# Performance work log

Measured on AMD Instinct MI355X. Metric: run time of the kernel, lower is better.

The kernel has to match this reference:

```python
import jax, jax.numpy as jnp
import numpy as np
from functools import partial

B, S, H = 4, 2048, 1152
NH, HD = 12, 96          # heads, head_dim
NM, MD = 4, 128          # memory heads (indices 6..9), mem_dim
K = 4                    # base kernel
STRIDE = 64              # NeuralMemory chunk stride
INNER = 4 * H            # GLU inner dim
CS_DIL = (1, 2, 4, 8, 16, 32)  # DilatedConvStack: config.dilations[:6]
HEAD_DIL = ((1, 2, 4), (1, 1, 1), (4, 8, 16), (8, 16, 32), (32, 64, 128),
            (64, 128, 256), (256, 512, 1024), (1, 100, 200), (1, 500, 1000),
            (1, 1024, 2048), (3, 9, 27), (5, 25, 125))
MEM_HEADS = (6, 7, 8, 9)


def setup_inputs() -> dict:
    key = jax.random.key(0)
    ks = iter(jax.random.split(key, 48))
    def nrm(shape, s=0.02):
        return jax.random.normal(next(ks), shape, jnp.float32) * s
    return {
        'x': jax.random.normal(next(ks), (B, S, H), jnp.float32),
        'norm1_w': jnp.ones((H,), jnp.float32),
        'norm2_w': jnp.ones((H,), jnp.float32),
        'norm3_w': jnp.ones((H,), jnp.float32),
        'cs_w': nrm((6, H, K), 0.1), 'cs_b': jnp.zeros((6, H), jnp.float32),
        'cs_proj_w': nrm((H, H)), 'cs_proj_b': jnp.zeros((H,), jnp.float32),
        'gate_proj_w': nrm((H, 2 * H)),
        'router_w': nrm((H, NH)), 'router_b': jnp.zeros((NH,), jnp.float32),
        'head_w': nrm((NH, 3, HD, K), 0.1), 'head_b': jnp.zeros((NH, 3, HD), jnp.float32),
        'mem_q': nrm((NM, HD, HD), 0.01), 'mem_k': nrm((NM, HD, HD), 0.01),
        'mem_v': nrm((NM, HD, MD), 0.01), 'mem_gw': nrm((NM, HD)),
        'mem_gb': jnp.full((NM,), -2.0, jnp.float32), 'mem_out': nrm((NM, MD, HD), 0.01),
        'mixgate_w': nrm((H, H)), 'mixgate_b': jnp.full((H,), 2.0, jnp.float32),
        'mixing_w': nrm((H, H)), 'mixing_b': jnp.zeros((H,), jnp.float32),
        'ffn_in_w': nrm((H, 2 * INNER)), 'ffn_out_w': nrm((INNER, H)),
        'cg_w': nrm((H,)), 'cg_b': jnp.float32(1.0),
        'sg_w': nrm((H,)), 'sg_b': jnp.float32(1.0),
        'fg_w': nrm((H,)), 'fg_b': jnp.float32(1.0),
    }


def rmsnorm(x, w, eps=1e-6):
    n = jax.lax.rsqrt(jnp.mean(x * x, axis=-1, keepdims=True) + eps)
    return x * n * w


def dconv(x, w, b, d):
    """Depthwise causal dilated conv. x:[B,S,C], w:[C,K], b:[C]."""
    s = x.shape[1]
    pad = (w.shape[1] - 1) * d
    xp = jnp.pad(x, ((0, 0), (pad, 0), (0, 0)))
    acc = b
    for j in range(w.shape[1]):
        acc = acc + w[:, j] * jax.lax.dynamic_slice_in_dim(xp, j * d, s, axis=1)
    return acc


def conv_stack(x, cs_w, cs_b, proj_w, proj_b):
    h = x
    for i, d in enumerate(CS_DIL):
        h = h + jax.nn.gelu(dconv(h, cs_w[i], cs_b[i], d), approximate=False)
    return h @ proj_w + proj_b


def neural_memory(xm, Wq, Wk, Wv, gw, gb, Wout):
    """Chunked fast-weight memory for NM heads at once. xm:[B,S,NM,HD]."""
    q = jnp.einsum('bsnd,nde->bsne', xm, Wq)
    k = jnp.einsum('bsnd,nde->bsne', xm, Wk)
    v = jnp.einsum('bsnd,ndm->bsnm', xm, Wv)
    g = jax.nn.sigmoid(jnp.einsum('bsnd,nd->bsn', xm, gw) + gb)[..., None]  # [B,S,NM,1]
    nC = S // STRIDE
    def chunk(a):  # [B,S,...] -> [nC,B,STRIDE,...]
        return a.reshape(B, nC, STRIDE, *a.shape[2:]).swapaxes(0, 1)
    q_c, kg_c, v_c = chunk(q), chunk(k * g), chunk(v)
    ga_c = chunk(g).mean(axis=2)[..., None]  # [nC,B,NM,1,1]
    M0 = jnp.zeros((B, NM, HD, MD), xm.dtype)
    def step(M, xs):
        qc, kc, vc, ga = xs
        reads = jnp.einsum('bsnd,bndm->bsnm', qc, M)
        write = jnp.einsum('bsnd,bsnm->bndm', kc, vc)
        return (1.0 - ga) * M + write, reads
    _, reads = jax.lax.scan(step, M0, (q_c, kg_c, v_c, ga_c))
    reads = reads.swapaxes(0, 1).reshape(B, S, NM, MD)
    return jnp.einsum('bsnm,nmd->bsnd', reads, Wout)


def multi_head_state(x, gate_proj_w, router_w, router_b, head_w, head_b,
                     mem_q, mem_k, mem_v, mem_gw, mem_gb, mem_out,
                     mixgate_w, mixgate_b, mixing_w, mixing_b):
    head_weights = jax.nn.sigmoid(x @ router_w + router_b)  # [B,S,NH]
    gp = x @ gate_proj_w
    xg = gp[..., :H] * jax.nn.sigmoid(gp[..., H:])
    xh = xg.reshape(B, S, NH, HD)
    outs = []
    for i in range(NH):
        h = xh[:, :, i, :]
        for j, d in enumerate(HEAD_DIL[i]):
            h = h + dconv(h, head_w[i, j], head_b[i, j], d)
        outs.append(h)
    mem = neural_memory(xh[:, :, MEM_HEADS[0]:MEM_HEADS[-1] + 1, :],
                        mem_q, mem_k, mem_v, mem_gw, mem_gb, mem_out)
    for n, i in enumerate(MEM_HEADS):
        outs[i] = outs[i] + mem[:, :, n, :]
    out = jnp.stack(outs, axis=2) * head_weights[..., None]
    out = out.reshape(B, S, H)
    out = out * jax.nn.sigmoid(out @ mixgate_w + mixgate_b)
    return out @ mixing_w + mixing_b


def glu(x, win, wout):
    h = x @ win
    return (h[..., :INNER] * jax.nn.sigmoid(h[..., INNER:])) @ wout


def reference(x, norm1_w, norm2_w, norm3_w, cs_w, cs_b, cs_proj_w, cs_proj_b,
              gate_proj_w, router_w, router_b, head_w, head_b,
              mem_q, mem_k, mem_v, mem_gw, mem_gb, mem_out,
              mixgate_w, mixgate_b, mixing_w, mixing_b,
              ffn_in_w, ffn_out_w, cg_w, cg_b, sg_w, sg_b, fg_w, fg_b):
    gc = jax.nn.sigmoid(x @ cg_w + cg_b)[..., None]
    x = x + gc * conv_stack(rmsnorm(x, norm1_w), cs_w, cs_b, cs_proj_w, cs_proj_b)
    gs = jax.nn.sigmoid(x @ sg_w + sg_b)[..., None]
    x = x + gs * multi_head_state(rmsnorm(x, norm2_w), gate_proj_w, router_w, router_b,
                                  head_w, head_b, mem_q, mem_k, mem_v, mem_gw, mem_gb,
                                  mem_out, mixgate_w, mixgate_b, mixing_w, mixing_b)
    gf = jax.nn.sigmoid(x @ fg_w + fg_b)[..., None]
    x = x + gf * glu(rmsnorm(x, norm3_w), ffn_in_w, ffn_out_w)
    return x
```

## Files before the change

### kernel.cpp

```cpp
#include <hip/hip_runtime.h>
#include <hip/hip_bf16.h>
#include <math.h>

#define TOKENS 8192
#define HDIM 1152
#define SEQ 2048
#define NHEADS 12
#define HEADD 96
#define NMEM 4
#define MEMD 128
#define FINNER 4608

typedef __hip_bfloat16 bf16;
typedef __attribute__((ext_vector_type(8))) short short8;
typedef __attribute__((ext_vector_type(4))) float floatx4;

__device__ __constant__ int g_hd_dil[NHEADS * 3] = {
    1, 2, 4,   1, 1, 1,    4, 8, 16,   8, 16, 32,
    32, 64, 128, 64, 128, 256, 256, 512, 1024, 1, 100, 200,
    1, 500, 1000, 1, 1024, 2048, 3, 9, 27, 5, 25, 125};

__device__ inline float sigm(float x) { return 1.0f / (1.0f + expf(-x)); }
__device__ inline float gelu_exact(float x) {
  return 0.5f * x * (1.0f + erff(x * 0.70710678118654752f));
}
__device__ inline float wred(float v) {
#pragma unroll
  for (int o = 32; o > 0; o >>= 1) v += __shfl_down(v, o);
  return v;
}
__device__ inline void gl_lds16(const bf16* g, bf16* l) {
  __builtin_amdgcn_global_load_lds(
      (const __attribute__((address_space(1))) unsigned int*)g,
      (__attribute__((address_space(3))) unsigned int*)l, 16, 0, 0);
}

__global__ __launch_bounds__(256) void k_transpose_bf16(
    const float* __restrict__ W, bf16* __restrict__ WT, int K, int N) {
  __shared__ float t[32][33];
  int k0 = blockIdx.y * 32, n0 = blockIdx.x * 32;
  int tx = threadIdx.x & 31, ty = threadIdx.x >> 5;
#pragma unroll
  for (int i = 0; i < 32; i += 8)
    t[ty + i][tx] = W[(size_t)(k0 + ty + i) * N + (n0 + tx)];
  __syncthreads();
#pragma unroll
  for (int i = 0; i < 32; i += 8)
    WT[(size_t)(n0 + ty + i) * K + (k0 + tx)] = __float2bfloat16(t[tx][ty + i]);
}

__global__ __launch_bounds__(256) void k_transpose_pair(
    const float* __restrict__ W, bf16* __restrict__ WT, int K, int N) {
  __shared__ float t[32][33];
  int half = N >> 1;
  int k0 = blockIdx.y * 32, n0 = blockIdx.x * 32;
  int tx = threadIdx.x & 31, ty = threadIdx.x >> 5;
  int c = (tx < 16) ? (n0 / 2 + tx) : (half + n0 / 2 + tx - 16);
#pragma unroll
  for (int i = 0; i < 32; i += 8)
    t[ty + i][tx] = W[(size_t)(k0 + ty + i) * N + c];
  __syncthreads();
#pragma unroll
  for (int i = 0; i < 32; i += 8) {
    int r = ty + i;
    int cc = (r >> 1) + (r & 1) * 16;
    WT[(size_t)(n0 + r) * K + (k0 + tx)] = __float2bfloat16(t[tx][cc]);
  }
}

__global__ __launch_bounds__(256) void k_rms_gate(
    const float* __restrict__ x, const float* __restrict__ nw,
    const float* __restrict__ gw, const float* __restrict__ gb,
    bf16* __restrict__ outb, float* __restrict__ gout,
    const float* __restrict__ rw, const float* __restrict__ rb,
    float* __restrict__ hwout) {
  int wave = threadIdx.x >> 6, lane = threadIdx.x & 63;
  int tok = blockIdx.x * 4 + wave;
  const float* row = x + (size_t)tok * HDIM;
  float2 a[9];
  float s2 = 0.f, gd = 0.f;
#pragma unroll
  for (int p = 0; p < 9; ++p) {
    int i2 = lane + 64 * p;
    a[p] = *reinterpret_cast<const float2*>(&row[i2 * 2]);
    float2 g2 = *reinterpret_cast<const float2*>(&gw[i2 * 2]);
    s2 += a[p].x * a[p].x + a[p].y * a[p].y;
    gd += a[p].x * g2.x + a[p].y * g2.y;
  }
  s2 = wred(s2);
  gd = wred(gd);
  if (lane == 0) gout[tok] = sigm(gd + gb[0]);
  s2 = __shfl(s2, 0);
  float rn = 1.0f / sqrtf(s2 / (float)HDIM + 1e-6f);
  float racc[NHEADS];
#pragma unroll
  for (int o = 0; o < NHEADS; ++o) racc[o] = 0.f;
#pragma unroll
  for (int p = 0; p < 9; ++p) {
    int i2 = lane + 64 * p;
    float2 w2 = *reinterpret_cast<const float2*>(&nw[i2 * 2]);
    float nx = a[p].x * rn * w2.x;
    float ny = a[p].y * rn * w2.y;
    __hip_bfloat162 pr;
    pr.x = __float2bfloat16(nx);
    pr.y = __float2bfloat16(ny);
    *reinterpret_cast<__hip_bfloat162*>(&outb[(size_t)tok * HDIM + i2 * 2]) = pr;
    if (hwout) {
      const float* rp = &rw[(size_t)(i2 * 2) * NHEADS];
#pragma unroll
      for (int o = 0; o < NHEADS; ++o)
        racc[o] += nx * rp[o] + ny * rp[NHEADS + o];
    }
  }
  if (hwout) {
#pragma unroll
    for (int o = 0; o < NHEADS; ++o) {
      float r = wred(racc[o]);
      if (lane == 0) hwout[(size_t)tok * NHEADS + o] = sigm(r + rb[o]);
    }
  }
}

#define CS_T 256
#define CS_HALO 189
#define CS_ROWS 445
#define CS_J 28
__global__ __launch_bounds__(256) void k_convstack(
    const bf16* __restrict__ hin, bf16* __restrict__ outb,
    const float* __restrict__ cw, const float* __restrict__ cb) {
  __shared__ float cur[CS_ROWS * 16];
  int bx = blockIdx.x;
  int cs = bx % 72;
  int tile = (bx / 72) & 7;
  int b = bx / 576;
  int c0 = cs * 16;
  int S0 = tile * CS_T;
  int tid = threadIdx.x;
  int c = tid & 15, pg = tid >> 4;
  for (int i = tid; i < CS_ROWS * 8; i += 256) {
    int p = i >> 3, cc2 = (i & 7) * 2;
    int sg = S0 - CS_HALO + p;
    if (sg >= 0) {
      unsigned int u = *reinterpret_cast<const unsigned int*>(
          &hin[((size_t)(b * SEQ + sg)) * HDIM + c0 + cc2]);
      cur[p * 16 + cc2] = __uint_as_float(u << 16);
      cur[p * 16 + cc2 + 1] = __uint_as_float(u & 0xffff0000u);
    } else {
      cur[p * 16 + cc2] = 0.f;
      cur[p * 16 + cc2 + 1] = 0.f;
    }
  }
  const int dil[6] = {1, 2, 4, 8, 16, 32};
  const int Nk[6] = {3, 9, 21, 45, 93, 189};
  float nv[CS_J];
#pragma unroll
  for (int k = 0; k < 6; ++k) {
    int d = dil[k];
    float w0 = cw[((size_t)k * HDIM + c0 + c) * 4 + 0];
    float w1 = cw[((size_t)k * HDIM + c0 + c) * 4 + 1];
    float w2 = cw[((size_t)k * HDIM + c0 + c) * 4 + 2];
    float w3 = cw[((size_t)k * HDIM + c0 + c) * 4 + 3];
    float bb = cb[(size_t)k * HDIM + c0 + c];
    __syncthreads();
#pragma unroll
    for (int j = 0; j < CS_J; ++j) {
      int p = pg + 16 * j;
      if (p >= Nk[k] && p < CS_ROWS) {
        int i = p * 16 + c;
        float acc = bb + w0 * cur[i - 3 * d * 16] + w1 * cur[i - 2 * d * 16] +
                    w2 * cur[i - d * 16] + w3 * cur[i];
        int sg = S0 - CS_HALO + p;
        nv[j] = (sg >= 0) ? (cur[i] + gelu_exact(acc)) : 0.f;
      }
    }
    __syncthreads();
#pragma unroll
    for (int j = 0; j < CS_J; ++j) {
      int p = pg + 16 * j;
      if (p >= Nk[k] && p < CS_ROWS) cur[p * 16 + c] = nv[j];
    }
  }
  __syncthreads();
  for (int r = pg; r < CS_T; r += 16) {
    outb[((size_t)(b * SEQ + S0 + r)) * HDIM + c0 + c] =
        __float2bfloat16(cur[(CS_HALO + r) * 16 + c]);
  }
}

__global__ __launch_bounds__(256) void k_headconv(
    const float* __restrict__ hin, float* __restrict__ hout,
    const float* __restrict__ hw_, const float* __restrict__ hb_, int j) {
  size_t idx4 = (size_t)blockIdx.x * 256 + threadIdx.x;
  if (idx4 >= (size_t)TOKENS * HDIM / 4) return;
  size_t idx = idx4 * 4;
  int c = (int)(idx % HDIM);
  int head = c / HEADD, hd = c % HEADD;
  size_t tok = idx / HDIM;
  int s = (int)(tok % SEQ);
  int d = g_hd_dil[head * 3 + j];
  const float4* wv = reinterpret_cast<const float4*>(
      hw_ + ((size_t)(head * 3 + j) * HEADD + hd) * 4);
  float4 w0 = wv[0], w1 = wv[1], w2 = wv[2], w3 = wv[3];
  float4 bb = *reinterpret_cast<const float4*>(
      &hb_[(size_t)(head * 3 + j) * HEADD + hd]);
  float av0 = bb.x, av1 = bb.y, av2 = bb.z, av3 = bb.w;
  float4 base = *reinterpret_cast<const float4*>(&hin[idx]);
#pragma unroll
  for (int jj = 0; jj < 4; ++jj) {
    int back = (3 - jj) * d;
    if (s - back >= 0) {
      float4 t = *reinterpret_cast<const float4*>(&hin[idx - (size_t)back * HDIM]);
      float a0 = (jj == 0) ? w0.x : (jj == 1) ? w0.y : (jj == 2) ? w0.z : w0.w;
      float a1 = (jj == 0) ? w1.x : (jj == 1) ? w1.y : (jj == 2) ? w1.z : w1.w;
      float a2 = (jj == 0) ? w2.x : (jj == 1) ? w2.y : (jj == 2) ? w2.z : w2.w;
      float a3 = (jj == 0) ? w3.x : (jj == 1) ? w3.y : (jj == 2) ? w3.z : w3.w;
      av0 += a0 * t.x;
      av1 += a1 * t.y;
      av2 += a2 * t.z;
      av3 += a3 * t.w;
    }
  }
  float4 o = {base.x + av0, base.y + av1, base.z + av2, base.w + av3};
  *reinterpret_cast<float4*>(&hout[idx]) = o;
}

template <int MODE>
__global__ __launch_bounds__(256) void k_gemm(
    const bf16* __restrict__ A, const bf16* __restrict__ BT,
    const float* __restrict__ bias, const float* __restrict__ gate,
    const float* addin, float* outf, bf16* outb, int M, int N, int K) {
  __shared__ bf16 As[128 * 64];
  __shared__ bf16 Bs[128 * 64];
  const int tid = threadIdx.x;
  const int m0 = blockIdx.y * 128, n0 = blockIdx.x * 128;
  const int wave = tid >> 6, lane = tid & 63;
  const int wm = (wave & 1) * 64, wn = (wave >> 1) * 64;
  const int l16 = lane & 15, kq = lane >> 4;
  const int srow = lane >> 3;
  const int schunk = ((lane & 7) - srow) & 7;
  const bf16* gA = A + (size_t)(m0 + wave * 32 + srow) * K + schunk * 8;
  const bf16* gB = BT + (size_t)(n0 + wave * 32 + srow) * K + schunk * 8;
  bf16* lA = &As[wave * 32 * 64];
  bf16* lB = &Bs[wave * 32 * 64];
  const size_t rstride = (size_t)8 * K;
  const int col0 = ((kq + l16) & 7) * 8;
  const int col1 = ((kq + 4 + l16) & 7) * 8;
  floatx4 acc[4][4];
  floatx4 zero = {0.f, 0.f, 0.f, 0.f};
#pragma unroll
  for (int i = 0; i < 4; ++i)
#pragma unroll
    for (int jj = 0; jj < 4; ++jj) acc[i][jj] = zero;

  for (int k0 = 0; k0 < K; k0 += 64) {
    __syncthreads();
#pragma unroll
    for (int i = 0; i < 4; ++i) {
      gl_lds16(gA + k0 + i * rstride, lA + i * 8 * 64);
      gl_lds16(gB + k0 + i * rstride, lB + i * 8 * 64);
    }
    __syncthreads();
#pragma unroll
    for (int ks = 0; ks < 2; ++ks) {
      const int col = ks ? col1 : col0;
      short8 af[4], bfr[4];
#pragma unroll
      for (int t = 0; t < 4; ++t) {
        af[t] = *reinterpret_cast<const short8*>(&As[(wm + t * 16 + l16) * 64 + col]);
        bfr[t] = *reinterpret_cast<const short8*>(&Bs[(wn + t * 16 + l16) * 64 + col]);
      }
#pragma unroll
      for (int mt = 0; mt < 4; ++mt)
#pragma unroll
        for (int nt = 0; nt < 4; ++nt)
          acc[mt][nt] = __builtin_amdgcn_mfma_f32_16x16x32_bf16(
              af[mt], bfr[nt], acc[mt][nt], 0, 0, 0);
    }
  }

  if (MODE == 4 || MODE == 5) {
    const int halfN = N >> 1;
#pragma unroll
    for (int mt = 0; mt < 4; ++mt) {
#pragma unroll
      for (int nt = 0; nt < 4; ++nt) {
        int nn = n0 + wn + nt * 16 + l16;
#pragma unroll
        for (int r = 0; r < 4; ++r) {
          float v = acc[mt][nt][r];
          float g = __shfl_xor(v, 1);
          if ((lane & 1) == 0) {
            int m = m0 + wm + mt * 16 + kq * 4 + r;
            float res = v * sigm(g);
            size_t o = (size_t)m * halfN + (nn >> 1);
            if (MODE == 4) outf[o] = res;
            else outb[o] = __float2bfloat16(res);
          }
        }
      }
    }
    return;
  }

#pragma unroll
  for (int mt = 0; mt < 4; ++mt) {
#pragma unroll
    for (int nt = 0; nt < 4; ++nt) {
      int n = n0 + wn + nt * 16 + l16;
      float bv = bias ? bias[n] : 0.f;
#pragma unroll
      for (int r = 0; r < 4; ++r) {
        int m = m0 + wm + mt * 16 + kq * 4 + r;
        float v = acc[mt][nt][r] + bv;
        size_t o = (size_t)m * N + n;
        if (MODE == 2) outf[o] = addin[o] + gate[m] * v;
        else if (MODE == 6) outb[o] = __float2bfloat16(addin[o] * sigm(v));
      }
    }
  }
}

#define QT 16
#define QTP 20
__global__ __launch_bounds__(256) void k_qkvg(
    const float* __restrict__ xh, const float* __restrict__ Wq,
    const float* __restrict__ Wk, const float* __restrict__ Wv,
    const float* __restrict__ gw, const float* __restrict__ gb,
    float* __restrict__ q, float* __restrict__ kg, float* __restrict__ v,
    float* __restrict__ gout) {
  __shared__ float xT[384 * QTP];
  __shared__ float gsh[QT][NMEM];
  int bx = blockIdx.x;
  int grp = bx & 1;
  int tile = bx >> 1;
  int t0 = tile * QT;
  int tid = threadIdx.x;
  for (int i = tid; i < 384 * QT; i += 256) {
    int t = i / 384, dd = i % 384;
    xT[dd * QTP + t] = xh[(size_t)(t0 + t) * HDIM + 6 * HEADD + dd];
  }
  __syncthreads();
  if (grp == 0) {
    if (tid < 64) {
      int t = tid >> 2, n = tid & 3;
      float a = gb[n];
      for (int d = 0; d < HEADD; ++d)
        a += xT[(n * HEADD + d) * QTP + t] * gw[n * HEADD + d];
      float s = sigm(a);
      gsh[t][n] = s;
      gout[(size_t)(t0 + t) * NMEM + n] = s;
    }
    __syncthreads();
  }
  int o = grp * 1024 + tid * 4;
  if (o >= 1280) return;
  float acc[4][QT];
#pragma unroll
  for (int e = 0; e < 4; ++e)
#pragma unroll
    for (int t = 0; t < QT; ++t) acc[e][t] = 0.f;

  if (o < 768) {
    int qk = (o >= 384) ? 1 : 0;
    int oo = o - qk * 384;
    int n = oo / HEADD, eb = oo % HEADD;
    const float* W = (qk ? Wk : Wq) + (size_t)n * HEADD * HEADD;
    const int ddb = n * HEADD;
    for (int d = 0; d < HEADD; ++d) {
      float4 w4 = *reinterpret_cast<const float4*>(&W[(size_t)d * HEADD + eb]);
      const float* xr = &xT[(ddb + d) * QTP];
#pragma unroll
      for (int tq = 0; tq < QT / 4; ++tq) {
        float4 xv = *reinterpret_cast<const float4*>(&xr[tq * 4]);
        float xa[4] = {xv.x, xv.y, xv.z, xv.w};
#pragma unroll
        for (int u = 0; u < 4; ++u) {
          acc[0][tq * 4 + u] += xa[u] * w4.x;
          acc[1][tq * 4 + u] += xa[u] * w4.y;
          acc[2][tq * 4 + u] += xa[u] * w4.z;
          acc[3][tq * 4 + u] += xa[u] * w4.w;
        }
      }
    }
    if (qk == 0) {
#pragma unroll
      for (int t = 0; t < QT; ++t) {
        float4 ov = {acc[0][t], acc[1][t], acc[2][t], acc[3][t]};
        *reinterpret_cast<float4*>(&q[(size_t)(t0 + t) * 384 + oo]) = ov;
      }
    } else {
#pragma unroll
      for (int t = 0; t < QT; ++t) {
        float g = gsh[t][n];
        float4 ov = {acc[0][t] * g, acc[1][t] * g, acc[2][t] * g, acc[3][t] * g};
        *reinterpret_cast<float4*>(&kg[(size_t)(t0 + t) * 384 + oo]) = ov;
      }
    }
  } else {
    int i2 = o - 768;
    int n = i2 / MEMD, eb = i2 % MEMD;
    const float* W = Wv + (size_t)n * HEADD * MEMD;
    const int ddb = n * HEADD;
    for (int d = 0; d < HEADD; ++d) {
      float4 w4 = *reinterpret_cast<const float4*>(&W[(size_t)d * MEMD + eb]);
      const float* xr = &xT[(ddb + d) * QTP];
#pragma unroll
      for (int tq = 0; tq < QT / 4; ++tq) {
        float4 xv = *reinterpret_cast<const float4*>(&xr[tq * 4]);
        float xa[4] = {xv.x, xv.y, xv.z, xv.w};
#pragma unroll
        for (int u = 0; u < 4; ++u) {
          acc[0][tq * 4 + u] += xa[u] * w4.x;
          acc[1][tq * 4 + u] += xa[u] * w4.y;
          acc[2][tq * 4 + u] += xa[u] * w4.z;
          acc[3][tq * 4 + u] += xa[u] * w4.w;
        }
      }
    }
#pragma unroll
    for (int t = 0; t < QT; ++t) {
      float4 ov = {acc[0][t], acc[1][t], acc[2][t], acc[3][t]};
      *reinterpret_cast<float4*>(&v[(size_t)(t0 + t) * 512 + i2]) = ov;
    }
  }
}

__global__ __launch_bounds__(256) void k_memW(const float* __restrict__ kg,
                                              const float* __restrict__ v,
                                              float* __restrict__ W) {
  __shared__ float X[64 * 96];
  __shared__ float V[64 * 128];
  int bx = blockIdx.x;
  int bn = bx >> 5, ch = bx & 31;
  int b = bn >> 2, n = bn & 3;
  int t0 = b * SEQ + ch * 64;
  int tid = threadIdx.x;
  for (int i = tid; i < 64 * 96; i += 256) {
    int s = i / 96, d = i % 96;
    X[i] = kg[((size_t)(t0 + s) * NMEM + n) * HEADD + d];
  }
  for (int i = tid; i < 64 * 128; i += 256) {
    int s = i >> 7, m = i & 127;
    V[i] = v[((size_t)(t0 + s) * NMEM + n) * MEMD + m];
  }
  __syncthreads();
  float* Wb = W + (size_t)bx * 96 * 128;
  for (int t = tid; t < 768; t += 256) {
    int d0 = (t >> 5) * 4, m0 = (t & 31) * 4;
    float acc[4][4] = {};
    for (int s = 0; s < 64; ++s) {
      float4 xv = *reinterpret_cast<const float4*>(&X[s * 96 + d0]);
      float4 vv = *reinterpret_cast<const float4*>(&V[s * 128 + m0]);
      float xa[4] = {xv.x, xv.y, xv.z, xv.w};
      float va[4] = {vv.x, vv.y, vv.z, vv.w};
#pragma unroll
      for (int a = 0; a < 4; ++a)
#pragma unroll
        for (int e = 0; e < 4; ++e) acc[a][e] += xa[a] * va[e];
    }
#pragma unroll
    for (int a = 0; a < 4; ++a) {
      float4 o = {acc[a][0], acc[a][1], acc[a][2], acc[a][3]};
      *reinterpret_cast<float4*>(&Wb[(size_t)(d0 + a) * 128 + m0]) = o;
    }
  }
}

__global__ __launch_bounds__(256) void k_memscanM(const float* __restrict__ W,
                                                  const float* __restrict__ g,
                                                  float* __restrict__ Mp) {
  __shared__ float ga_sh[32];
  int bx = blockIdx.x;
  int bn = bx / 48, j = bx % 48;
  int elem = j * 256 + threadIdx.x;
  int b = bn >> 2, n = bn & 3;
  int tid = threadIdx.x;
  {
    int ch = tid >> 3, i8 = tid & 7;
    float s = 0.f;
#pragma unroll
    for (int t = 0; t < 8; ++t)
      s += g[((size_t)b * SEQ + ch * 64 + i8 * 8 + t) * NMEM + n];
#pragma unroll
    for (int o = 4; o > 0; o >>= 1) s += __shfl_down(s, o);
    if (i8 == 0) ga_sh[ch] = s * (1.0f / 64.0f);
  }
  __syncthreads();
  float wreg[32];
  size_t base0 = (size_t)bn * 32 * 12288 + elem;
#pragma unroll
  for (int ch = 0; ch < 32; ++ch) wreg[ch] = W[base0 + (size_t)ch * 12288];
  float M = 0.f;
#pragma unroll
  for (int ch = 0; ch < 32; ++ch) {
    Mp[base0 + (size_t)ch * 12288] = M;
    M = (1.f - ga_sh[ch]) * M + wreg[ch];
  }
}

__global__ __launch_bounds__(256) void k_memR(const float* __restrict__ q,
                                              const float* __restrict__ Mp,
                                              float* __restrict__ rd) {
  extern __shared__ float smem[];
  float* Q = smem;
  float* Ms = smem + 64 * 96;
  int bx = blockIdx.x;
  int bn = bx >> 5, ch = bx & 31;
  int b = bn >> 2, n = bn & 3;
  int t0 = b * SEQ + ch * 64;
  int tid = threadIdx.x;
  for (int i = tid; i < 64 * 96; i += 256) {
    int s = i / 96, d = i % 96;
    Q[i] = q[((size_t)(t0 + s) * NMEM + n) * HEADD + d];
  }
  for (int i = tid; i < 96 * 128; i += 256)
    Ms[i] = Mp[((size_t)bn * 32 + ch) * 12288 + i];
  __syncthreads();
  for (int t = tid; t < 512; t += 256) {
    int s0 = (t >> 5) * 4, m0 = (t & 31) * 4;
    float acc[4][4] = {};
    for (int k = 0; k < 96; ++k) {
      float4 mv = *reinterpret_cast<const float4*>(&Ms[k * 128 + m0]);
      float ma[4] = {mv.x, mv.y, mv.z, mv.w};
#pragma unroll
      for (int si = 0; si < 4; ++si) {
        float qs = Q[(s0 + si) * 96 + k];
#pragma unroll
        for (int mi = 0; mi < 4; ++mi) acc[si][mi] += qs * ma[mi];
      }
    }
#pragma unroll
    for (int si = 0; si < 4; ++si) {
      float4 o = {acc[si][0], acc[si][1], acc[si][2], acc[si][3]};
      *reinterpret_cast<float4*>(
          &rd[((size_t)(t0 + s0 + si) * NMEM + n) * MEMD + m0]) = o;
    }
  }
}

__global__ __launch_bounds__(256) void k_combine(
    const float* __restrict__ hconv, const float* __restrict__ reads,
    const float* __restrict__ Wout, const float* __restrict__ hw,
    float* __restrict__ outf, bf16* __restrict__ outb) {
  __shared__ float rd[NMEM * MEMD];
  int tok = blockIdx.x, tid = threadIdx.x;
  for (int i = tid; i < NMEM * MEMD; i += 256)
    rd[i] = reads[(size_t)tok * NMEM * MEMD + i];
  __syncthreads();
  for (int c = tid; c < HDIM; c += 256) {
    int head = c / HEADD, hd = c % HEADD;
    float v = hconv[(size_t)tok * HDIM + c];
    if (head >= 6 && head < 10) {
      int n = head - 6;
      const float* W = Wout + (size_t)(n * MEMD) * HEADD + hd;
      for (int m2 = 0; m2 < MEMD; ++m2) v += rd[n * MEMD + m2] * W[(size_t)m2 * HEADD];
    }
    v *= hw[tok * NHEADS + head];
    outf[(size_t)tok * HDIM + c] = v;
    outb[(size_t)tok * HDIM + c] = __float2bfloat16(v);
  }
}

extern "C" void kernel_launch(void* const* d_in, const int* in_sizes, int n_in,
                              void* d_out, int out_size, void* d_ws,
                              size_t ws_size, hipStream_t stream) {
  const float* x_in = (const float*)d_in[0];
  const float* norm1_w = (const float*)d_in[1];
  const float* norm2_w = (const float*)d_in[2];
  const float* norm3_w = (const float*)d_in[3];
  const float* cs_w = (const float*)d_in[4];
  const float* cs_b = (const float*)d_in[5];
  const float* cs_proj_w = (const float*)d_in[6];
  const float* cs_proj_b = (const float*)d_in[7];
  const float* gate_proj_w = (const float*)d_in[8];
  const float* router_w = (const float*)d_in[9];
  const float* router_b = (const float*)d_in[10];
  const float* head_w = (const float*)d_in[11];
  const float* head_b = (const float*)d_in[12];
  const float* mem_q = (const float*)d_in[13];
  const float* mem_k = (const float*)d_in[14];
  const float* mem_v = (const float*)d_in[15];
  const float* mem_gw = (const float*)d_in[16];
  const float* mem_gb = (const float*)d_in[17];
  const float* mem_out = (const float*)d_in[18];
  const float* mixgate_w = (const float*)d_in[19];
  const float* mixgate_b = (const float*)d_in[20];
  const float* mixing_w = (const float*)d_in[21];
  const float* mixing_b = (const float*)d_in[22];
  const float* ffn_in_w = (const float*)d_in[23];
  const float* ffn_out_w = (const float*)d_in[24];
  const float* cg_w = (const float*)d_in[25];
  const float* cg_b = (const float*)d_in[26];
  const float* sg_w = (const float*)d_in[27];
  const float* sg_b = (const float*)d_in[28];
  const float* fg_w = (const float*)d_in[29];
  const float* fg_b = (const float*)d_in[30];
  float* out = (float*)d_out;

  char* wsp = (char*)d_ws;
  size_t off = 0;
  auto alloc = [&](size_t bytes) -> char* {
    char* p = wsp + off;
    off += (bytes + 255) & ~(size_t)255;
    return p;
  };
  bf16* NB = (bf16*)alloc((size_t)TOKENS * HDIM * 2);
  float* F1 = (float*)alloc((size_t)TOKENS * HDIM * 4);
  float* F2 = (float*)alloc((size_t)TOKENS * HDIM * 4);
  float* F3 = (float*)alloc((size_t)TOKENS * HDIM * 4);
  char* REG = alloc((size_t)TOKENS * FINNER * 2);
  float* qb = (float*)REG;
  float* kgb = (float*)(REG + (size_t)TOKENS * 384 * 4);
  float* vb = (float*)((char*)kgb + (size_t)TOKENS * 384 * 4);
  float* rdb = (float*)((char*)vb + (size_t)TOKENS * 512 * 4);
  bf16* XG = (bf16*)REG;
  bf16* NB2 = (bf16*)REG;
  bf16* NBc = (bf16*)REG;
  bf16* WTcs = (bf16*)alloc((size_t)1152 * 1152 * 2);
  bf16* WTgp = (bf16*)alloc((size_t)2304 * 1152 * 2);
  bf16* WTmg = (bf16*)alloc((size_t)1152 * 1152 * 2);
  bf16* WTmx = (bf16*)alloc((size_t)1152 * 1152 * 2);
  float* G1 = (float*)alloc(TOKENS * 4);
  float* G2 = (float*)alloc(TOKENS * 4);
  float* G3 = (float*)alloc(TOKENS * 4);
  float* GM = (float*)alloc((size_t)TOKENS * NMEM * 4);
  float* HW = (float*)alloc((size_t)TOKENS * NHEADS * 4);
  bf16* WTfin = (bf16*)F1;
  bf16* WTfout = (bf16*)F2;
  float* Wbuf = F2;
  float* Mpref = F3;

  const int gE4 = (TOKENS * HDIM) / (4 * 256);

  k_transpose_bf16<<<dim3(36, 36), 256, 0, stream>>>(cs_proj_w, WTcs, 1152, 1152);
  k_transpose_pair<<<dim3(72, 36), 256, 0, stream>>>(gate_proj_w, WTgp, 1152, 2304);
  k_transpose_bf16<<<dim3(36, 36), 256, 0, stream>>>(mixgate_w, WTmg, 1152, 1152);
  k_transpose_bf16<<<dim3(36, 36), 256, 0, stream>>>(mixing_w, WTmx, 1152, 1152);

  k_rms_gate<<<2048, 256, 0, stream>>>(x_in, norm1_w, cg_w, cg_b, NB, G1,
                                       nullptr, nullptr, nullptr);
  k_convstack<<<2304, 256, 0, stream>>>(NB, NBc, cs_w, cs_b);
  k_gemm<2><<<dim3(9, 64), 256, 0, stream>>>(NBc, WTcs, cs_proj_b, G1, x_in, out,
                                             nullptr, TOKENS, 1152, 1152);

  k_rms_gate<<<2048, 256, 0, stream>>>(out, norm2_w, sg_w, sg_b, NB, G2,
                                       router_w, router_b, HW);
  k_gemm<4><<<dim3(18, 64), 256, 0, stream>>>(NB, WTgp, nullptr, nullptr, nullptr,
                                              F3, nullptr, TOKENS, 2304, 1152);
  k_headconv<<<gE4, 256, 0, stream>>>(F3, F1, head_w, head_b, 0);
  k_headconv<<<gE4, 256, 0, stream>>>(F1, F2, head_w, head_b, 1);
  k_headconv<<<gE4, 256, 0, stream>>>(F2, F1, head_w, head_b, 2);
  k_qkvg<<<1024, 256, 0, stream>>>(F3, mem_q, mem_k, mem_v, mem_gw, mem_gb,
                                   qb, kgb, vb, GM);
  k_memW<<<512, 256, 0, stream>>>(kgb, vb, Wbuf);
  k_memscanM<<<768, 256, 0, stream>>>(Wbuf, GM, Mpref);
  k_memR<<<512, 256, (64 * 96 + 96 * 128) * 4, stream>>>(qb, Mpref, rdb);
  k_combine<<<TOKENS, 256, 0, stream>>>(F1, rdb, mem_out, HW, F2, NB);
  k_gemm<6><<<dim3(9, 64), 256, 0, stream>>>(NB, WTmg, mixgate_b, nullptr, F2,
                                             nullptr, NB2, TOKENS, 1152, 1152);
  k_gemm<2><<<dim3(9, 64), 256, 0, stream>>>(NB2, WTmx, mixing_b, G2, out, out,
                                             nullptr, TOKENS, 1152, 1152);

  k_rms_gate<<<2048, 256, 0, stream>>>(out, norm3_w, fg_w, fg_b, NB, G3,
                                       nullptr, nullptr, nullptr);
  k_transpose_pair<<<dim3(288, 36), 256, 0, stream>>>(ffn_in_w, WTfin, 1152, 9216);
  k_transpose_bf16<<<dim3(36, 144), 256, 0, stream>>>(ffn_out_w, WTfout, 4608, 1152);
  k_gemm<5><<<dim3(72, 64), 256, 0, stream>>>(NB, WTfin, nullptr, nullptr, nullptr,
                                              nullptr, XG, TOKENS, 9216, 1152);
  k_gemm<2><<<dim3(9, 64), 256, 0, stream>>>(XG, WTfout, nullptr, G3, out, out,
                                             nullptr, TOKENS, 1152, 4608);
}
```

Baseline: 1.241 ms.

## Fuse memory output projection into k_memR and vectorize k_combine

Moves the per-token memory read output projection (reads @ mem_out) out of k_combine and into k_memR, where the 64x128 read tile is staged in shared memory and multiplied by mem_out per chunk. k_combine becomes a simple float4 elementwise kernel that adds the projected read, scales by the head weight, and writes the fp32 and bf16 outputs. The aim is to remove the scalar, poorly parallel 128-long dot products per channel in k_combine, where only 4 of 12 heads did work per token. The trade-off is that the projection in k_memR reads mem_out from global memory without caching it, and the kernel holds more live accumulators.

```diff
diff --git a/kernel.cpp b/kernel.cpp
--- a/kernel.cpp
+++ b/kernel.cpp
@@ -500,7 +500,8 @@
 
 __global__ __launch_bounds__(256) void k_memR(const float* __restrict__ q,
                                               const float* __restrict__ Mp,
-                                              float* __restrict__ rd) {
+                                              const float* __restrict__ Wout,
+                                              float* __restrict__ rdp) {
   extern __shared__ float smem[];
   float* Q = smem;
   float* Ms = smem + 64 * 96;
@@ -516,9 +517,15 @@
   for (int i = tid; i < 96 * 128; i += 256)
     Ms[i] = Mp[((size_t)bn * 32 + ch) * 12288 + i];
   __syncthreads();
-  for (int t = tid; t < 512; t += 256) {
+  float acc[2][4][4];
+#pragma unroll
+  for (int tt = 0; tt < 2; ++tt) {
+    int t = tid + tt * 256;
     int s0 = (t >> 5) * 4, m0 = (t & 31) * 4;
-    float acc[4][4] = {};
+#pragma unroll
+    for (int si = 0; si < 4; ++si)
+#pragma unroll
+      for (int mi = 0; mi < 4; ++mi) acc[tt][si][mi] = 0.f;
     for (int k = 0; k < 96; ++k) {
       float4 mv = *reinterpret_cast<const float4*>(&Ms[k * 128 + m0]);
       float ma[4] = {mv.x, mv.y, mv.z, mv.w};
@@ -526,39 +533,73 @@
       for (int si = 0; si < 4; ++si) {
         float qs = Q[(s0 + si) * 96 + k];
 #pragma unroll
-        for (int mi = 0; mi < 4; ++mi) acc[si][mi] += qs * ma[mi];
-      }
-    }
+        for (int mi = 0; mi < 4; ++mi) acc[tt][si][mi] += qs * ma[mi];
+      }
+    }
+  }
+  __syncthreads();
+  float* reads_s = smem;
+#pragma unroll
+  for (int tt = 0; tt < 2; ++tt) {
+    int t = tid + tt * 256;
+    int s0 = (t >> 5) * 4, m0 = (t & 31) * 4;
 #pragma unroll
     for (int si = 0; si < 4; ++si) {
-      float4 o = {acc[si][0], acc[si][1], acc[si][2], acc[si][3]};
-      *reinterpret_cast<float4*>(
-          &rd[((size_t)(t0 + s0 + si) * NMEM + n) * MEMD + m0]) = o;
-    }
+      float4 o = {acc[tt][si][0], acc[tt][si][1], acc[tt][si][2], acc[tt][si][3]};
+      *reinterpret_cast<float4*>(&reads_s[(s0 + si) * 128 + m0]) = o;
+    }
+  }
+  __syncthreads();
+  const float* Wn = Wout + (size_t)n * MEMD * HEADD;
+  for (int it = tid; it < 64 * 24; it += 256) {
+    int s = it / 24, c4 = (it % 24) * 4;
+    float p0 = 0.f, p1 = 0.f, p2 = 0.f, p3 = 0.f;
+    for (int m = 0; m < MEMD; ++m) {
+      float rv = reads_s[s * 128 + m];
+      float4 w4 = *reinterpret_cast<const float4*>(&Wn[(size_t)m * HEADD + c4]);
+      p0 += rv * w4.x;
+      p1 += rv * w4.y;
+      p2 += rv * w4.z;
+      p3 += rv * w4.w;
+    }
+    float4 o = {p0, p1, p2, p3};
+    *reinterpret_cast<float4*>(
+        &rdp[((size_t)(t0 + s) * NMEM + n) * HEADD + c4]) = o;
   }
 }
 
 __global__ __launch_bounds__(256) void k_combine(
-    const float* __restrict__ hconv, const float* __restrict__ reads,
-    const float* __restrict__ Wout, const float* __restrict__ hw,
-    float* __restrict__ outf, bf16* __restrict__ outb) {
-  __shared__ float rd[NMEM * MEMD];
-  int tok = blockIdx.x, tid = threadIdx.x;
-  for (int i = tid; i < NMEM * MEMD; i += 256)
-    rd[i] = reads[(size_t)tok * NMEM * MEMD + i];
-  __syncthreads();
-  for (int c = tid; c < HDIM; c += 256) {
-    int head = c / HEADD, hd = c % HEADD;
-    float v = hconv[(size_t)tok * HDIM + c];
-    if (head >= 6 && head < 10) {
-      int n = head - 6;
-      const float* W = Wout + (size_t)(n * MEMD) * HEADD + hd;
-      for (int m2 = 0; m2 < MEMD; ++m2) v += rd[n * MEMD + m2] * W[(size_t)m2 * HEADD];
-    }
-    v *= hw[tok * NHEADS + head];
-    outf[(size_t)tok * HDIM + c] = v;
-    outb[(size_t)tok * HDIM + c] = __float2bfloat16(v);
-  }
+    const float* __restrict__ hconv, const float* __restrict__ rdp,
+    const float* __restrict__ hw, float* __restrict__ outf,
+    bf16* __restrict__ outb) {
+  size_t idx4 = (size_t)blockIdx.x * 256 + threadIdx.x;
+  if (idx4 >= (size_t)TOKENS * HDIM / 4) return;
+  size_t idx = idx4 * 4;
+  int c = (int)(idx % HDIM);
+  size_t tok = idx / HDIM;
+  int head = c / HEADD, hd = c % HEADD;
+  float4 v = *reinterpret_cast<const float4*>(&hconv[idx]);
+  if (head >= 6 && head < 10) {
+    float4 r = *reinterpret_cast<const float4*>(
+        &rdp[((size_t)tok * NMEM + (head - 6)) * HEADD + hd]);
+    v.x += r.x;
+    v.y += r.y;
+    v.z += r.z;
+    v.w += r.w;
+  }
+  float w = hw[tok * NHEADS + head];
+  v.x *= w;
+  v.y *= w;
+  v.z *= w;
+  v.w *= w;
+  *reinterpret_cast<float4*>(&outf[idx]) = v;
+  __hip_bfloat162 p01, p23;
+  p01.x = __float2bfloat16(v.x);
+  p01.y = __float2bfloat16(v.y);
+  p23.x = __float2bfloat16(v.z);
+  p23.y = __float2bfloat16(v.w);
+  *reinterpret_cast<__hip_bfloat162*>(&outb[idx]) = p01;
+  *reinterpret_cast<__hip_bfloat162*>(&outb[idx + 2]) = p23;
 }
 
 extern "C" void kernel_launch(void* const* d_in, const int* in_sizes, int n_in,
@@ -654,8 +695,8 @@
                                    qb, kgb, vb, GM);
   k_memW<<<512, 256, 0, stream>>>(kgb, vb, Wbuf);
   k_memscanM<<<768, 256, 0, stream>>>(Wbuf, GM, Mpref);
-  k_memR<<<512, 256, (64 * 96 + 96 * 128) * 4, stream>>>(qb, Mpref, rdb);
-  k_combine<<<TOKENS, 256, 0, stream>>>(F1, rdb, mem_out, HW, F2, NB);
+  k_memR<<<512, 256, (64 * 96 + 96 * 128) * 4, stream>>>(qb, Mpref, mem_out, rdb);
+  k_combine<<<gE4, 256, 0, stream>>>(F1, rdb, HW, F2, NB);
   k_gemm<6><<<dim3(9, 64), 256, 0, stream>>>(NB, WTmg, mixgate_b, nullptr, F2,
                                              nullptr, NB2, TOKENS, 1152, 1152);
   k_gemm<2><<<dim3(9, 64), 256, 0, stream>>>(NB2, WTmx, mixing_b, G2, out, out,
```

New measurement: 1.215 ms. -2.1%, faster.
